# Kernel tuning notes

Hardware: AMD Instinct MI355X
Metric: run time of the kernel (lower is better)

## Reference

```python
import jax, jax.numpy as jnp
import numpy as np
import math

# Config constants (match init_kwargs)
E = 8          # n_experts
TOPK = 2       # attn_topk
DIM = 1024     # transformer_dim
B = 4          # batch_size
S = 1024       # max_seq_len
H = 1024       # num_heads * head_dim
SCALE = 1.0 / math.sqrt(DIM)  # original divides scores by sqrt(self.dim)


def setup_inputs() -> dict:
    key = jax.random.key(0)
    ks = jax.random.split(key, 8)
    w = 0.02  # weight init scale
    return {
        "X": jax.random.normal(ks[0], (B, S, DIM), jnp.float32),
        "mask": jnp.ones((B, S), jnp.float32),
        "switch_W": jax.random.normal(ks[1], (DIM * S, E), jnp.float32) * w,
        "switch_b": jnp.zeros((E,), jnp.float32),
        "Wq": jax.random.normal(ks[2], (E, DIM, H), jnp.float32) * w,
        "bq": jnp.zeros((E, H), jnp.float32),
        "Wk": jax.random.normal(ks[3], (E, DIM, H), jnp.float32) * w,
        "bk": jnp.zeros((E, H), jnp.float32),
        "Wv": jax.random.normal(ks[4], (E, DIM, H), jnp.float32) * w,
        "bv": jnp.zeros((E, H), jnp.float32),
        "Wff": jax.random.normal(ks[5], (E, H, DIM), jnp.float32) * w,
        "bff": jnp.zeros((E, DIM), jnp.float32),
    }


def _dispatch_mask(route_prob):
    # top-k expert routing per batch element -> hard {0,1} mask [B, E]
    _, idx = jax.lax.top_k(route_prob, TOPK)  # [B, TOPK]
    b = route_prob.shape[0]
    return jnp.zeros((b, E), route_prob.dtype).at[jnp.arange(b)[:, None], idx].set(1.0)


def reference(X, mask, switch_W, switch_b, Wq, bq, Wk, bk, Wv, bv, Wff, bff):
    b, s, d = X.shape
    # Router: Linear(dim*seq_len -> n_experts) + softmax; preprocess -> idx_list
    logits = X.reshape(b, -1) @ switch_W + switch_b          # [B, E]
    route_prob = jax.nn.softmax(logits, axis=-1)
    m = _dispatch_mask(route_prob)                            # [B, E] dispatch mask (idx_list)

    # Per-expert Q/K/V projections (ColumnParallelLinearWithMoE over routed batches)
    Q = jnp.einsum('bsd,edh->ebsh', X, Wq) + bq[:, None, None, :]  # [E,B,S,H]
    K = jnp.einsum('bsd,edh->ebsh', X, Wk) + bk[:, None, None, :]
    V = jnp.einsum('bsd,edh->ebsh', X, Wv) + bv[:, None, None, :]

    # RowParallelMatmulWithMoE: per-expert scores, softmax (dropout p=0)
    scores = jnp.einsum('ebsh,ebth->ebst', Q, K) * SCALE      # [E,B,S,S]
    P = jax.nn.softmax(scores, axis=-1)

    # index_add_ combine of per-expert attn maps (second preprocess reuses same routing)
    A = jnp.einsum('be,ebst->bst', m, P)                      # [B,S,S]

    # ColumnParallelMatmulWithMoE: attn @ V per expert
    ctx = jnp.einsum('bst,ebth->ebsh', A, V)                  # [E,B,S,H]

    # RowParallelLinearWithMoE output projection, then index_add_ combine
    out = jnp.einsum('ebsh,ehd->ebsd', ctx, Wff) + bff[:, None, None, :]
    y = jnp.einsum('be,ebsd->bsd', m, out)                    # [B,S,DIM]
    return y
```

## Files before the change

kernel.cpp:

```cpp
#include <hip/hip_runtime.h>
#include <math.h>

typedef unsigned short u16;
typedef __attribute__((ext_vector_type(8))) short bffrag;
typedef __attribute__((ext_vector_type(4))) float f32x4;
typedef __attribute__((ext_vector_type(4))) unsigned short us4;
typedef __attribute__((ext_vector_type(8))) unsigned short us8;

#define SCALE_QK (1.0f/32.0f)

__device__ __forceinline__ u16 f2bf(float f) {
    unsigned u = __builtin_bit_cast(unsigned, f);
    u += 0x7fffu + ((u >> 16) & 1u);
    return (u16)(u >> 16);
}

__device__ __forceinline__ void gld16(const u16* g, u16* l) {
    __builtin_amdgcn_global_load_lds(
        (const __attribute__((address_space(1))) void*)g,
        (__attribute__((address_space(3))) void*)l, 16, 0, 0);
}

__global__ __launch_bounds__(256) void router_partial(const float* __restrict__ X,
                                                      const float* __restrict__ sW,
                                                      float* __restrict__ part) {
    float acc[32];
    #pragma unroll
    for (int a = 0; a < 32; ++a) acc[a] = 0.f;
    int tid = blockIdx.x * 256 + threadIdx.x;
    #pragma unroll
    for (int q = 0; q < 4; ++q) {
        int i = tid + q * 262144;
        float4 w0 = *(const float4*)(sW + (size_t)i * 8);
        float4 w1 = *(const float4*)(sW + (size_t)i * 8 + 4);
        #pragma unroll
        for (int b = 0; b < 4; ++b) {
            float x = X[((size_t)b << 20) + i];
            acc[b*8+0] += x * w0.x; acc[b*8+1] += x * w0.y;
            acc[b*8+2] += x * w0.z; acc[b*8+3] += x * w0.w;
            acc[b*8+4] += x * w1.x; acc[b*8+5] += x * w1.y;
            acc[b*8+6] += x * w1.z; acc[b*8+7] += x * w1.w;
        }
    }
    __shared__ float wsum[4][32];
    int lane = threadIdx.x & 63, wv = threadIdx.x >> 6;
    #pragma unroll
    for (int a = 0; a < 32; ++a) {
        float v = acc[a];
        #pragma unroll
        for (int off = 32; off; off >>= 1) v += __shfl_down(v, off, 64);
        if (lane == 0) wsum[wv][a] = v;
    }
    __syncthreads();
    int t = threadIdx.x;
    if (t < 32)
        part[(size_t)t * 1024 + blockIdx.x] = wsum[0][t] + wsum[1][t] + wsum[2][t] + wsum[3][t];
}

__global__ __launch_bounds__(256) void router_final(const float* __restrict__ part,
                                                    const float* __restrict__ sb,
                                                    int* __restrict__ sel_need) {
    __shared__ float ps[32][8];
    __shared__ float lg[32];
    int t = threadIdx.x, a = t >> 3, c = t & 7;
    {
        float s = 0.f;
        const float* p = part + (size_t)a * 1024 + c * 128;
        for (int i = 0; i < 128; ++i) s += p[i];
        ps[a][c] = s;
    }
    __syncthreads();
    if (t < 32) {
        float v = 0.f;
        #pragma unroll
        for (int j = 0; j < 8; ++j) v += ps[t][j];
        lg[t] = v + sb[t & 7];
    }
    __syncthreads();
    if (t < 4) {
        int base = t * 8;
        int e1 = 0; float v1 = lg[base];
        for (int e = 1; e < 8; ++e) { if (lg[base + e] > v1) { v1 = lg[base + e]; e1 = e; } }
        int e2 = -1; float v2 = -INFINITY;
        for (int e = 0; e < 8; ++e) {
            if (e == e1) continue;
            if (lg[base + e] > v2) { v2 = lg[base + e]; e2 = e; }
        }
        sel_need[t * 2] = e1; sel_need[t * 2 + 1] = e2;
    }
    __syncthreads();
    if (t < 8) {
        int need = 0;
        for (int j = 0; j < 8; ++j) need |= (sel_need[j] == t);
        sel_need[8 + t] = need;
    }
}

__global__ __launch_bounds__(256) void c1_partial(const float* __restrict__ Wff,
        const float* __restrict__ bv, const int* __restrict__ sel_need,
        float* __restrict__ cpart) {
    int e = blockIdx.z;
    if (!sel_need[8 + e]) return;
    int d = blockIdx.x * 256 + threadIdx.x;
    int h0 = blockIdx.y * 128;
    const float* W = Wff + ((size_t)e << 20) + (size_t)h0 * 1024 + d;
    const float* bvp = bv + e * 1024 + h0;
    float s = 0.f;
    #pragma unroll 4
    for (int h = 0; h < 128; ++h) s += bvp[h] * W[(size_t)h * 1024];
    cpart[(e * 8 + blockIdx.y) * 1024 + d] = s;
}

__global__ __launch_bounds__(256) void ybias_kernel(const float* __restrict__ cpart,
        const float* __restrict__ bff, const int* __restrict__ sel,
        float* __restrict__ ybias) {
    int b = blockIdx.y;
    int d = blockIdx.x * 256 + threadIdx.x;
    int e0 = sel[b * 2], e1 = sel[b * 2 + 1];
    float c0 = 0.f, c1v = 0.f;
    #pragma unroll
    for (int hc = 0; hc < 8; ++hc) {
        c0  += cpart[(e0 * 8 + hc) * 1024 + d];
        c1v += cpart[(e1 * 8 + hc) * 1024 + d];
    }
    ybias[b * 1024 + d] = 2.f * (c0 + c1v) + bff[e0 * 1024 + d] + bff[e1 * 1024 + d];
}

__global__ __launch_bounds__(256) void cvt_misc(const float* __restrict__ X,
                                                const float* __restrict__ Wv,
                                                const int* __restrict__ sel_need,
                                                u16* __restrict__ Xb, u16* __restrict__ WvB) {
    int yz = blockIdx.y;
    const float* src; u16* dst;
    if (yz < 4) {
        src = X + ((size_t)yz << 20);  dst = Xb + ((size_t)yz << 20);
    } else {
        int e = yz - 4;
        if (!sel_need[8 + e]) return;
        src = Wv + ((size_t)e << 20);  dst = WvB + ((size_t)e << 20);
    }
    size_t i = (size_t)(blockIdx.x * 256 + threadIdx.x) * 8;
    float4 a = *(const float4*)(src + i);
    float4 b = *(const float4*)(src + i + 4);
    us8 o;
    o[0] = f2bf(a.x); o[1] = f2bf(a.y); o[2] = f2bf(a.z); o[3] = f2bf(a.w);
    o[4] = f2bf(b.x); o[5] = f2bf(b.y); o[6] = f2bf(b.z); o[7] = f2bf(b.w);
    *(us8*)(dst + i) = o;
}

__global__ __launch_bounds__(256) void cvt_wt(const float* __restrict__ Wq,
                                              const float* __restrict__ Wk,
                                              const float* __restrict__ Wff,
                                              const float* __restrict__ X,
                                              const int* __restrict__ sel_need,
                                              u16* __restrict__ WqT, u16* __restrict__ WkT,
                                              u16* __restrict__ WffT, u16* __restrict__ XbT) {
    int z = blockIdx.z;
    int type = z >> 3, e = z & 7;
    const float* src;
    u16* dst;
    if (type < 3) {
        if (!sel_need[8 + e]) return;
        src = (type == 0 ? Wq : type == 1 ? Wk : Wff) + ((size_t)e << 20);
        dst = (type == 0 ? WqT : type == 1 ? WkT : WffT) + ((size_t)e << 20);
    } else {
        int b = z & 3;
        src = X + ((size_t)b << 20);
        dst = XbT + ((size_t)b << 20);
    }
    __shared__ u16 lt[128 * 136];
    int R0 = blockIdx.y * 128, C0 = blockIdx.x * 128;
    int t = threadIdx.x;
    int c = t & 127;
    int rh = (t >> 7) * 4;
    #pragma unroll
    for (int it = 0; it < 16; ++it) {
        int r4 = it * 8 + rh;
        us4 o;
        #pragma unroll
        for (int j = 0; j < 4; ++j)
            o[j] = f2bf(src[(size_t)(R0 + r4 + j) * 1024 + C0 + c]);
        *(us4*)&lt[c * 136 + r4] = o;
    }
    __syncthreads();
    int dd = (t & 15) * 8;
    int hh = t >> 4;
    #pragma unroll
    for (int it = 0; it < 8; ++it) {
        int cr = it * 16 + hh;
        us8 o = *(const us8*)&lt[cr * 136 + dd];
        *(us8*)(dst + (size_t)(C0 + cr) * 1024 + R0 + dd) = o;
    }
}

__device__ __forceinline__ void stage_half8(const u16* g, int ld, u16* ldst, int tid) {
    int r = tid >> 3;
    int j = ((tid ^ r) & 7) * 8;
    gld16(g + (size_t)r * ld + j, ldst + tid * 8);
    gld16(g + (size_t)(r + 64) * ld + j, ldst + 4096 + tid * 8);
}

template<int Q, bool LASTVM>
__device__ __forceinline__ void phase8(const u16* Ac, const bffrag (&bfr)[4][2],
                                       f32x4 (&acc)[8][4], int rb, int l15, int x0,
                                       const u16* sg, int sld, u16* sdst, int tid) {
    bffrag af[2][2];
    #pragma unroll
    for (int mm = 0; mm < 2; ++mm) {
        int r = (rb + Q * 32 + mm * 16 + l15) * 64;
        af[mm][0] = *(const bffrag*)(Ac + r + x0);
        af[mm][1] = *(const bffrag*)(Ac + r + (x0 ^ 32));
    }
    __builtin_amdgcn_sched_barrier(0);
    stage_half8(sg, sld, sdst, tid);
    __builtin_amdgcn_sched_barrier(0);
    __builtin_amdgcn_s_barrier();
    asm volatile("s_waitcnt lgkmcnt(0)" ::: "memory");
    __builtin_amdgcn_sched_barrier(0);
    __builtin_amdgcn_s_setprio(1);
    #pragma unroll
    for (int ks = 0; ks < 2; ++ks)
        #pragma unroll
        for (int mm = 0; mm < 2; ++mm)
            #pragma unroll
            for (int nn = 0; nn < 4; ++nn)
                acc[Q*2+mm][nn] = __builtin_amdgcn_mfma_f32_16x16x32_bf16(
                    af[mm][ks], bfr[nn][ks], acc[Q*2+mm][nn], 0, 0, 0);
    __builtin_amdgcn_s_setprio(0);
    __builtin_amdgcn_sched_barrier(0);
    if (LASTVM) asm volatile("s_waitcnt vmcnt(4)" ::: "memory");
    __builtin_amdgcn_s_barrier();
}

__device__ __forceinline__ void gemm8(const u16* __restrict__ A, int lda,
                                      const u16* __restrict__ B, int ldb,
                                      int K, f32x4 (&acc)[8][4]) {
    __shared__ u16 lds[65536];
    const int tid = threadIdx.x, l = tid & 63, wid = tid >> 6;
    const int wr = wid >> 2, wc = wid & 3;
    const int l15 = l & 15;
    const int rb = wr * 128;
    const int cb = wc * 64;
    const int x0 = (((l >> 4) ^ (l & 7)) * 8);
    const int m0 = blockIdx.y * 256, n0 = blockIdx.x * 256;
    const int nt = K >> 6;

    const u16* Ag = A + (size_t)m0 * lda;
    const u16* Bg = B + (size_t)n0 * ldb;

    stage_half8(Ag,                          lda, lds,                 tid);
    stage_half8(Ag + (size_t)128 * lda,      lda, lds + 8192,          tid);
    stage_half8(Bg,                          ldb, lds + 16384,         tid);
    stage_half8(Bg + (size_t)128 * ldb,      ldb, lds + 16384 + 8192,  tid);
    stage_half8(Bg + 64,                     ldb, lds + 32768 + 16384, tid);
    stage_half8(Bg + 64 + (size_t)128 * ldb, ldb, lds + 32768 + 16384 + 8192, tid);
    asm volatile("s_waitcnt vmcnt(4)" ::: "memory");
    __builtin_amdgcn_s_barrier();

    for (int t7 = 0; t7 < nt; ++t7) {
        const int cur = t7 & 1;
        u16* Ac = lds + cur * 32768;
        u16* Bc = Ac + 16384;
        u16* An = lds + (cur ^ 1) * 32768;
        const int ka = (t7 + 1 < nt ? t7 + 1 : nt - 1) << 6;
        const int kb = (t7 + 2 < nt ? t7 + 2 : nt - 1) << 6;
        const u16* sA0 = Ag + ka;
        const u16* sA1 = Ag + (size_t)128 * lda + ka;
        const u16* sB0 = Bg + kb;
        const u16* sB1 = Bg + (size_t)128 * ldb + kb;

        bffrag bfr[4][2];
        #pragma unroll
        for (int nn = 0; nn < 4; ++nn) {
            int r = (cb + nn * 16 + l15) * 64;
            bfr[nn][0] = *(const bffrag*)(Bc + r + x0);
            bfr[nn][1] = *(const bffrag*)(Bc + r + (x0 ^ 32));
        }
        phase8<0, false>(Ac, bfr, acc, rb, l15, x0, sA0, lda, An, tid);
        phase8<1, false>(Ac, bfr, acc, rb, l15, x0, sA1, lda, An + 8192, tid);
        phase8<2, false>(Ac, bfr, acc, rb, l15, x0, sB0, ldb, Bc, tid);
        phase8<3, true >(Ac, bfr, acc, rb, l15, x0, sB1, ldb, Bc + 8192, tid);
    }
}

__device__ __forceinline__ void zero8(f32x4 (&acc)[8][4]) {
    #pragma unroll
    for (int m = 0; m < 8; ++m)
        #pragma unroll
        for (int n = 0; n < 4; ++n)
            #pragma unroll
            for (int i = 0; i < 4; ++i) acc[m][n][i] = 0.f;
}

__device__ __forceinline__ void epi8_bf16(u16* __restrict__ C, int ldc,
                                          const f32x4 (&acc)[8][4],
                                          const float* __restrict__ biasN) {
    const int tid = threadIdx.x, l = tid & 63, wid = tid >> 6;
    const int wr = wid >> 2, wc = wid & 3;
    const int m0 = blockIdx.y * 256 + wr * 128, n0 = blockIdx.x * 256 + wc * 64;
    const int l15 = l & 15, l4 = (l >> 4) * 4;
    #pragma unroll
    for (int mt = 0; mt < 8; ++mt)
        #pragma unroll
        for (int nn = 0; nn < 4; ++nn) {
            int col = n0 + nn * 16 + l15;
            float bn = biasN ? biasN[col] : 0.f;
            #pragma unroll
            for (int i = 0; i < 4; ++i) {
                int row = m0 + mt * 16 + l4 + i;
                C[(size_t)row * ldc + col] = f2bf(acc[mt][nn][i] + bn);
            }
        }
}

__device__ __forceinline__ void epi8_f32(float* __restrict__ C, int ldc, float scale,
                                         const f32x4 (&acc)[8][4]) {
    const int tid = threadIdx.x, l = tid & 63, wid = tid >> 6;
    const int wr = wid >> 2, wc = wid & 3;
    const int m0 = blockIdx.y * 256 + wr * 128, n0 = blockIdx.x * 256 + wc * 64;
    const int l15 = l & 15, l4 = (l >> 4) * 4;
    #pragma unroll
    for (int mt = 0; mt < 8; ++mt)
        #pragma unroll
        for (int nn = 0; nn < 4; ++nn) {
            int col = n0 + nn * 16 + l15;
            #pragma unroll
            for (int i = 0; i < 4; ++i) {
                int row = m0 + mt * 16 + l4 + i;
                C[(size_t)row * ldc + col] = acc[mt][nn][i] * scale;
            }
        }
}

__global__ __launch_bounds__(512) void mfma8_qk(const u16* __restrict__ Xb,
        const u16* __restrict__ WqT, const u16* __restrict__ WkT,
        const float* __restrict__ bq, const float* __restrict__ bk,
        const int* __restrict__ sel, u16* __restrict__ Qb, u16* __restrict__ Kb) {
    int z = blockIdx.z, w = z >> 3, bs = z & 7;
    int b = bs >> 1, e = sel[bs];
    f32x4 acc[8][4]; zero8(acc);
    gemm8(Xb + ((size_t)b << 20), 1024, (w ? WkT : WqT) + ((size_t)e << 20), 1024, 1024, acc);
    epi8_bf16((w ? Kb : Qb) + ((size_t)bs << 20), 1024, acc, (w ? bk : bq) + e * 1024);
}

__global__ __launch_bounds__(512) void mfma8_sw(const u16* __restrict__ Qb,
        const u16* __restrict__ Kb, const u16* __restrict__ WffT,
        const u16* __restrict__ WvB, const int* __restrict__ sel,
        float* __restrict__ S, float* __restrict__ P0, float* __restrict__ P1) {
    int z = blockIdx.z;
    f32x4 acc[8][4]; zero8(acc);
    if (z < 8) {
        gemm8(Qb + ((size_t)z << 20), 1024, Kb + ((size_t)z << 20), 1024, 1024, acc);
        epi8_f32(S + ((size_t)z << 20), 1024, SCALE_QK, acc);
    } else {
        int h = (z >= 12), b = z & 3, e = sel[b * 2 + h];
        gemm8(WffT + ((size_t)e << 20), 1024, WvB + ((size_t)e << 20), 1024, 1024, acc);
        epi8_f32((h ? P1 : P0) + ((size_t)b << 20), 1024, 1.0f, acc);
    }
}

__global__ __launch_bounds__(256) void wvfadd(const float* __restrict__ P0,
                                              const float* __restrict__ P1,
                                              u16* __restrict__ W) {
    size_t i = (size_t)(blockIdx.x * 256 + threadIdx.x) * 8;
    float4 a0 = *(const float4*)(P0 + i),     a1 = *(const float4*)(P0 + i + 4);
    float4 b0 = *(const float4*)(P1 + i),     b1 = *(const float4*)(P1 + i + 4);
    us8 o;
    o[0] = f2bf(a0.x + b0.x); o[1] = f2bf(a0.y + b0.y);
    o[2] = f2bf(a0.z + b0.z); o[3] = f2bf(a0.w + b0.w);
    o[4] = f2bf(a1.x + b1.x); o[5] = f2bf(a1.y + b1.y);
    o[6] = f2bf(a1.z + b1.z); o[7] = f2bf(a1.w + b1.w);
    *(us8*)(W + i) = o;
}

__device__ __forceinline__ void stage_tile(const u16* a0, const u16* a1,
                                           const u16* b0, const u16* b1,
                                           u16* sa, u16* sb, int tid) {
    gld16(a0, &sa[tid * 8]);
    gld16(a1, &sa[2048 + tid * 8]);
    gld16(b0, &sb[tid * 8]);
    gld16(b1, &sb[2048 + tid * 8]);
}

__device__ __forceinline__ void gemm_ds(const u16* __restrict__ A, int lda,
                                        const u16* __restrict__ B, int ldb,
                                        int K, f32x4 (&acc)[4][4]) {
    __shared__ u16 sA[2][4096];
    __shared__ u16 sB[2][4096];
    const int tid = threadIdx.x, lane = tid & 63, wv = tid >> 6;
    const int wr = (wv >> 1) * 64, wc = (wv & 1) * 64;
    const int l15 = lane & 15, lk = (lane >> 4) * 8;
    const int m0 = blockIdx.y * 128, n0 = blockIdx.x * 128;
    const int r0 = tid >> 2, k8 = (tid & 3) * 8;

    const u16* a0 = A + (size_t)(m0 + r0) * lda + k8;
    const u16* a1 = A + (size_t)(m0 + 64 + r0) * lda + k8;
    const u16* b0 = B + (size_t)(n0 + r0) * ldb + k8;
    const u16* b1 = B + (size_t)(n0 + 64 + r0) * ldb + k8;

    stage_tile(a0, a1, b0, b1, sA[0], sB[0], tid);
    __syncthreads();

    const int nt = K >> 5;
    for (int t = 0; t < nt; ++t) {
        const int cur = t & 1;
        if (t + 1 < nt) {
            int k0 = (t + 1) << 5;
            stage_tile(a0 + k0, a1 + k0, b0 + k0, b1 + k0, sA[cur ^ 1], sB[cur ^ 1], tid);
        }
        bffrag av[4], bf[4];
        #pragma unroll
        for (int m = 0; m < 4; ++m)
            av[m] = *reinterpret_cast<const bffrag*>(&sA[cur][(wr + m * 16 + l15) * 32 + lk]);
        #pragma unroll
        for (int n = 0; n < 4; ++n)
            bf[n] = *reinterpret_cast<const bffrag*>(&sB[cur][(wc + n * 16 + l15) * 32 + lk]);
        #pragma unroll
        for (int m = 0; m < 4; ++m)
            #pragma unroll
            for (int n = 0; n < 4; ++n)
                acc[m][n] = __builtin_amdgcn_mfma_f32_16x16x32_bf16(av[m], bf[n], acc[m][n], 0, 0, 0);
        __syncthreads();
    }
}

__device__ __forceinline__ void zero_acc(f32x4 (&acc)[4][4]) {
    #pragma unroll
    for (int m = 0; m < 4; ++m)
        #pragma unroll
        for (int n = 0; n < 4; ++n)
            #pragma unroll
            for (int i = 0; i < 4; ++i) acc[m][n][i] = 0.f;
}

__device__ __forceinline__ void epilogue_bf16(u16* __restrict__ C, int ldc,
                                              const f32x4 (&acc)[4][4]) {
    const int tid = threadIdx.x, lane = tid & 63, wv = tid >> 6;
    const int wr = (wv >> 1) * 64, wc = (wv & 1) * 64;
    const int m0 = blockIdx.y * 128, n0 = blockIdx.x * 128;
    const int l15 = lane & 15, l4 = (lane >> 4) * 4;
    #pragma unroll
    for (int m = 0; m < 4; ++m)
        #pragma unroll
        for (int n = 0; n < 4; ++n) {
            int col = n0 + wc + n * 16 + l15;
            #pragma unroll
            for (int i = 0; i < 4; ++i) {
                int row = m0 + wr + m * 16 + l4 + i;
                C[(size_t)row * ldc + col] = f2bf(acc[m][n][i]);
            }
        }
}

__device__ __forceinline__ void epilogue_f32(float* __restrict__ C, int ldc,
                                             const f32x4 (&acc)[4][4],
                                             const float* __restrict__ bias1) {
    const int tid = threadIdx.x, lane = tid & 63, wv = tid >> 6;
    const int wr = (wv >> 1) * 64, wc = (wv & 1) * 64;
    const int m0 = blockIdx.y * 128, n0 = blockIdx.x * 128;
    const int l15 = lane & 15, l4 = (lane >> 4) * 4;
    #pragma unroll
    for (int m = 0; m < 4; ++m)
        #pragma unroll
        for (int n = 0; n < 4; ++n) {
            int col = n0 + wc + n * 16 + l15;
            float bn = bias1 ? bias1[col] : 0.f;
            #pragma unroll
            for (int i = 0; i < 4; ++i) {
                int row = m0 + wr + m * 16 + l4 + i;
                C[(size_t)row * ldc + col] = acc[m][n][i] + bn;
            }
        }
}

__global__ __launch_bounds__(256) void sm_combine(const float* __restrict__ S, u16* __restrict__ Ab) {
    int bs = blockIdx.x, b = bs >> 10, s = bs & 1023;
    const float* S0 = S + ((size_t)(b * 2) << 20) + (size_t)s * 1024;
    const float* S1 = S0 + (1u << 20);
    int t = threadIdx.x, lane = t & 63, wv = t >> 6;
    float4 x0 = *(const float4*)(S0 + t * 4);
    float4 x1 = *(const float4*)(S1 + t * 4);
    float m0 = fmaxf(fmaxf(x0.x, x0.y), fmaxf(x0.z, x0.w));
    float m1 = fmaxf(fmaxf(x1.x, x1.y), fmaxf(x1.z, x1.w));
    #pragma unroll
    for (int off = 32; off; off >>= 1) {
        m0 = fmaxf(m0, __shfl_xor(m0, off, 64));
        m1 = fmaxf(m1, __shfl_xor(m1, off, 64));
    }
    __shared__ float wred[4][4];
    if (lane == 0) { wred[wv][0] = m0; wred[wv][1] = m1; }
    __syncthreads();
    m0 = fmaxf(fmaxf(wred[0][0], wred[1][0]), fmaxf(wred[2][0], wred[3][0]));
    m1 = fmaxf(fmaxf(wred[0][1], wred[1][1]), fmaxf(wred[2][1], wred[3][1]));
    float4 e0, e1;
    e0.x = __expf(x0.x - m0); e0.y = __expf(x0.y - m0); e0.z = __expf(x0.z - m0); e0.w = __expf(x0.w - m0);
    e1.x = __expf(x1.x - m1); e1.y = __expf(x1.y - m1); e1.z = __expf(x1.z - m1); e1.w = __expf(x1.w - m1);
    float s0 = e0.x + e0.y + e0.z + e0.w;
    float s1 = e1.x + e1.y + e1.z + e1.w;
    #pragma unroll
    for (int off = 32; off; off >>= 1) {
        s0 += __shfl_xor(s0, off, 64);
        s1 += __shfl_xor(s1, off, 64);
    }
    if (lane == 0) { wred[wv][2] = s0; wred[wv][3] = s1; }
    __syncthreads();
    s0 = wred[0][2] + wred[1][2] + wred[2][2] + wred[3][2];
    s1 = wred[0][3] + wred[1][3] + wred[2][3] + wred[3][3];
    float r0 = 1.f / s0, r1 = 1.f / s1;
    us4 o;
    o[0] = f2bf(e0.x * r0 + e1.x * r1); o[1] = f2bf(e0.y * r0 + e1.y * r1);
    o[2] = f2bf(e0.z * r0 + e1.z * r1); o[3] = f2bf(e0.w * r0 + e1.w * r1);
    *(us4*)(Ab + ((size_t)b << 20) + (size_t)s * 1024 + t * 4) = o;
}

__global__ __launch_bounds__(256) void mfma_ax(const u16* __restrict__ Abf,
        const u16* __restrict__ XbT, u16* __restrict__ AXbf) {
    int b = blockIdx.z;
    f32x4 acc[4][4]; zero_acc(acc);
    gemm_ds(Abf + ((size_t)b << 20), 1024, XbT + ((size_t)b << 20), 1024, 1024, acc);
    epilogue_bf16(AXbf + ((size_t)b << 20), 1024, acc);
}

__global__ __launch_bounds__(256) void mfma_y(const u16* __restrict__ AXbf,
        const u16* __restrict__ Wvfsum, const float* __restrict__ ybias,
        float* __restrict__ y) {
    int b = blockIdx.z;
    f32x4 acc[4][4]; zero_acc(acc);
    gemm_ds(AXbf + ((size_t)b << 20), 1024, Wvfsum + ((size_t)b << 20), 1024, 1024, acc);
    epilogue_f32(y + ((size_t)b << 20), 1024, acc, ybias + b * 1024);
}

extern "C" void kernel_launch(void* const* d_in, const int* in_sizes, int n_in,
                              void* d_out, int out_size, void* d_ws, size_t ws_size,
                              hipStream_t stream) {
    const float* X   = (const float*)d_in[0];
    const float* sW  = (const float*)d_in[2];
    const float* sb  = (const float*)d_in[3];
    const float* Wq  = (const float*)d_in[4];
    const float* bq  = (const float*)d_in[5];
    const float* Wk  = (const float*)d_in[6];
    const float* bk  = (const float*)d_in[7];
    const float* Wv  = (const float*)d_in[8];
    const float* bv  = (const float*)d_in[9];
    const float* Wff = (const float*)d_in[10];
    const float* bff = (const float*)d_in[11];
    float* y = (float*)d_out;

    char* w = (char*)d_ws;
    float* part  = (float*)w;
    float* cpart = (float*)w;
    int*   sel   = (int*)(w + (1u << 18));
    float* ybias = (float*)(w + (1u << 18) + 256);
    u16* base = (u16*)(w + (1u << 19));
    u16* Xb   = base;
    u16* XbT  = Xb   + (4u << 20);
    u16* WqT  = XbT  + (4u << 20);
    u16* WkT  = WqT  + (8u << 20);
    u16* WffT = WkT  + (8u << 20);
    u16* WvB  = WffT + (8u << 20);
    u16* Qb   = WvB  + (8u << 20);
    u16* Kb   = Qb   + (8u << 20);
    float* S  = (float*)(Kb + (8u << 20));
    float* P0 = S  + (8u << 20);
    float* P1 = P0 + (4u << 20);
    u16* Wvfsum = Xb;
    u16* Abf    = WqT;
    u16* AXbf   = WkT;

    router_partial<<<1024, 256, 0, stream>>>(X, sW, part);
    router_final<<<1, 256, 0, stream>>>(part, sb, sel);
    c1_partial<<<dim3(4, 8, 8), 256, 0, stream>>>(Wff, bv, sel, cpart);
    ybias_kernel<<<dim3(4, 4), 256, 0, stream>>>(cpart, bff, sel, ybias);
    cvt_misc<<<dim3(512, 12), 256, 0, stream>>>(X, Wv, sel, Xb, WvB);
    cvt_wt<<<dim3(8, 8, 28), 256, 0, stream>>>(Wq, Wk, Wff, X, sel, WqT, WkT, WffT, XbT);

    mfma8_qk<<<dim3(4, 4, 16), 512, 0, stream>>>(Xb, WqT, WkT, bq, bk, sel, Qb, Kb);
    mfma8_sw<<<dim3(4, 4, 16), 512, 0, stream>>>(Qb, Kb, WffT, WvB, sel, S, P0, P1);
    wvfadd<<<2048, 256, 0, stream>>>(P0, P1, Wvfsum);
    sm_combine<<<4096, 256, 0, stream>>>(S, Abf);
    mfma_ax<<<dim3(8, 8, 4), 256, 0, stream>>>(Abf, XbT, AXbf);
    mfma_y<<<dim3(8, 8, 4), 256, 0, stream>>>(AXbf, Wvfsum, ybias, y);
}
```

Baseline: 239.1 us.

## Reassociate A·X·Wvf product, store scores/partials in bf16, drop X transpose

Reorders the final product from (A·X)·Wvfsum to A·(X·Wvfsum)^T-style by computing a per-batch Mt = Wvfsum·X first. That removes the need for a transposed bf16 copy of X, so the cvt_wt grid shrinks. Score matrices and the Wff·Wv partial products are now written as bf16 instead of fp32, halving their store and reload traffic in softmax and wvfadd. In exchange the scores are rounded to bf16 before softmax, which costs accuracy.

Result: faster. 221.8 us (-7.2%).

```diff
diff --git a/kernel.cpp b/kernel.cpp
--- a/kernel.cpp
+++ b/kernel.cpp
@@ -13,6 +13,10 @@
     unsigned u = __builtin_bit_cast(unsigned, f);
     u += 0x7fffu + ((u >> 16) & 1u);
     return (u16)(u >> 16);
+}
+__device__ __forceinline__ float bf2f(u16 v) {
+    unsigned u = ((unsigned)v) << 16;
+    return __builtin_bit_cast(float, u);
 }
 
 __device__ __forceinline__ void gld16(const u16* g, u16* l) {
@@ -151,23 +155,14 @@
 __global__ __launch_bounds__(256) void cvt_wt(const float* __restrict__ Wq,
                                               const float* __restrict__ Wk,
                                               const float* __restrict__ Wff,
-                                              const float* __restrict__ X,
                                               const int* __restrict__ sel_need,
                                               u16* __restrict__ WqT, u16* __restrict__ WkT,
-                                              u16* __restrict__ WffT, u16* __restrict__ XbT) {
+                                              u16* __restrict__ WffT) {
     int z = blockIdx.z;
     int type = z >> 3, e = z & 7;
-    const float* src;
-    u16* dst;
-    if (type < 3) {
-        if (!sel_need[8 + e]) return;
-        src = (type == 0 ? Wq : type == 1 ? Wk : Wff) + ((size_t)e << 20);
-        dst = (type == 0 ? WqT : type == 1 ? WkT : WffT) + ((size_t)e << 20);
-    } else {
-        int b = z & 3;
-        src = X + ((size_t)b << 20);
-        dst = XbT + ((size_t)b << 20);
-    }
+    if (!sel_need[8 + e]) return;
+    const float* src = (type == 0 ? Wq : type == 1 ? Wk : Wff) + ((size_t)e << 20);
+    u16* dst = (type == 0 ? WqT : type == 1 ? WkT : WffT) + ((size_t)e << 20);
     __shared__ u16 lt[128 * 136];
     int R0 = blockIdx.y * 128, C0 = blockIdx.x * 128;
     int t = threadIdx.x;
@@ -292,7 +287,7 @@
             for (int i = 0; i < 4; ++i) acc[m][n][i] = 0.f;
 }
 
-__device__ __forceinline__ void epi8_bf16(u16* __restrict__ C, int ldc,
+__device__ __forceinline__ void epi8_bf16(u16* __restrict__ C, int ldc, float scale,
                                           const f32x4 (&acc)[8][4],
                                           const float* __restrict__ biasN) {
     const int tid = threadIdx.x, l = tid & 63, wid = tid >> 6;
@@ -308,26 +303,7 @@
             #pragma unroll
             for (int i = 0; i < 4; ++i) {
                 int row = m0 + mt * 16 + l4 + i;
-                C[(size_t)row * ldc + col] = f2bf(acc[mt][nn][i] + bn);
-            }
-        }
-}
-
-__device__ __forceinline__ void epi8_f32(float* __restrict__ C, int ldc, float scale,
-                                         const f32x4 (&acc)[8][4]) {
-    const int tid = threadIdx.x, l = tid & 63, wid = tid >> 6;
-    const int wr = wid >> 2, wc = wid & 3;
-    const int m0 = blockIdx.y * 256 + wr * 128, n0 = blockIdx.x * 256 + wc * 64;
-    const int l15 = l & 15, l4 = (l >> 4) * 4;
-    #pragma unroll
-    for (int mt = 0; mt < 8; ++mt)
-        #pragma unroll
-        for (int nn = 0; nn < 4; ++nn) {
-            int col = n0 + nn * 16 + l15;
-            #pragma unroll
-            for (int i = 0; i < 4; ++i) {
-                int row = m0 + mt * 16 + l4 + i;
-                C[(size_t)row * ldc + col] = acc[mt][nn][i] * scale;
+                C[(size_t)row * ldc + col] = f2bf(acc[mt][nn][i] * scale + bn);
             }
         }
 }
@@ -340,36 +316,34 @@
     int b = bs >> 1, e = sel[bs];
     f32x4 acc[8][4]; zero8(acc);
     gemm8(Xb + ((size_t)b << 20), 1024, (w ? WkT : WqT) + ((size_t)e << 20), 1024, 1024, acc);
-    epi8_bf16((w ? Kb : Qb) + ((size_t)bs << 20), 1024, acc, (w ? bk : bq) + e * 1024);
+    epi8_bf16((w ? Kb : Qb) + ((size_t)bs << 20), 1024, 1.0f, acc, (w ? bk : bq) + e * 1024);
 }
 
 __global__ __launch_bounds__(512) void mfma8_sw(const u16* __restrict__ Qb,
         const u16* __restrict__ Kb, const u16* __restrict__ WffT,
         const u16* __restrict__ WvB, const int* __restrict__ sel,
-        float* __restrict__ S, float* __restrict__ P0, float* __restrict__ P1) {
+        u16* __restrict__ Sb, u16* __restrict__ P0b, u16* __restrict__ P1b) {
     int z = blockIdx.z;
     f32x4 acc[8][4]; zero8(acc);
     if (z < 8) {
         gemm8(Qb + ((size_t)z << 20), 1024, Kb + ((size_t)z << 20), 1024, 1024, acc);
-        epi8_f32(S + ((size_t)z << 20), 1024, SCALE_QK, acc);
+        epi8_bf16(Sb + ((size_t)z << 20), 1024, SCALE_QK, acc, nullptr);
     } else {
         int h = (z >= 12), b = z & 3, e = sel[b * 2 + h];
         gemm8(WffT + ((size_t)e << 20), 1024, WvB + ((size_t)e << 20), 1024, 1024, acc);
-        epi8_f32((h ? P1 : P0) + ((size_t)b << 20), 1024, 1.0f, acc);
-    }
-}
-
-__global__ __launch_bounds__(256) void wvfadd(const float* __restrict__ P0,
-                                              const float* __restrict__ P1,
+        epi8_bf16((h ? P1b : P0b) + ((size_t)b << 20), 1024, 1.0f, acc, nullptr);
+    }
+}
+
+__global__ __launch_bounds__(256) void wvfadd(const u16* __restrict__ P0b,
+                                              const u16* __restrict__ P1b,
                                               u16* __restrict__ W) {
     size_t i = (size_t)(blockIdx.x * 256 + threadIdx.x) * 8;
-    float4 a0 = *(const float4*)(P0 + i),     a1 = *(const float4*)(P0 + i + 4);
-    float4 b0 = *(const float4*)(P1 + i),     b1 = *(const float4*)(P1 + i + 4);
+    us8 a = *(const us8*)(P0b + i);
+    us8 b = *(const us8*)(P1b + i);
     us8 o;
-    o[0] = f2bf(a0.x + b0.x); o[1] = f2bf(a0.y + b0.y);
-    o[2] = f2bf(a0.z + b0.z); o[3] = f2bf(a0.w + b0.w);
-    o[4] = f2bf(a1.x + b1.x); o[5] = f2bf(a1.y + b1.y);
-    o[6] = f2bf(a1.z + b1.z); o[7] = f2bf(a1.w + b1.w);
+    #pragma unroll
+    for (int j = 0; j < 8; ++j) o[j] = f2bf(bf2f(a[j]) + bf2f(b[j]));
     *(us8*)(W + i) = o;
 }
 
@@ -473,15 +447,18 @@
         }
 }
 
-__global__ __launch_bounds__(256) void sm_combine(const float* __restrict__ S, u16* __restrict__ Ab) {
+__global__ __launch_bounds__(256) void sm_combine(const u16* __restrict__ Sb, u16* __restrict__ Ab) {
     int bs = blockIdx.x, b = bs >> 10, s = bs & 1023;
-    const float* S0 = S + ((size_t)(b * 2) << 20) + (size_t)s * 1024;
-    const float* S1 = S0 + (1u << 20);
+    const u16* S0 = Sb + ((size_t)(b * 2) << 20) + (size_t)s * 1024;
+    const u16* S1 = S0 + (1u << 20);
     int t = threadIdx.x, lane = t & 63, wv = t >> 6;
-    float4 x0 = *(const float4*)(S0 + t * 4);
-    float4 x1 = *(const float4*)(S1 + t * 4);
-    float m0 = fmaxf(fmaxf(x0.x, x0.y), fmaxf(x0.z, x0.w));
-    float m1 = fmaxf(fmaxf(x1.x, x1.y), fmaxf(x1.z, x1.w));
+    us4 xv0 = *(const us4*)(S0 + t * 4);
+    us4 xv1 = *(const us4*)(S1 + t * 4);
+    float x0[4], x1[4];
+    #pragma unroll
+    for (int j = 0; j < 4; ++j) { x0[j] = bf2f(xv0[j]); x1[j] = bf2f(xv1[j]); }
+    float m0 = fmaxf(fmaxf(x0[0], x0[1]), fmaxf(x0[2], x0[3]));
+    float m1 = fmaxf(fmaxf(x1[0], x1[1]), fmaxf(x1[2], x1[3]));
     #pragma unroll
     for (int off = 32; off; off >>= 1) {
         m0 = fmaxf(m0, __shfl_xor(m0, off, 64));
@@ -492,11 +469,11 @@
     __syncthreads();
     m0 = fmaxf(fmaxf(wred[0][0], wred[1][0]), fmaxf(wred[2][0], wred[3][0]));
     m1 = fmaxf(fmaxf(wred[0][1], wred[1][1]), fmaxf(wred[2][1], wred[3][1]));
-    float4 e0, e1;
-    e0.x = __expf(x0.x - m0); e0.y = __expf(x0.y - m0); e0.z = __expf(x0.z - m0); e0.w = __expf(x0.w - m0);
-    e1.x = __expf(x1.x - m1); e1.y = __expf(x1.y - m1); e1.z = __expf(x1.z - m1); e1.w = __expf(x1.w - m1);
-    float s0 = e0.x + e0.y + e0.z + e0.w;
-    float s1 = e1.x + e1.y + e1.z + e1.w;
+    float e0[4], e1[4];
+    #pragma unroll
+    for (int j = 0; j < 4; ++j) { e0[j] = __expf(x0[j] - m0); e1[j] = __expf(x1[j] - m1); }
+    float s0 = e0[0] + e0[1] + e0[2] + e0[3];
+    float s1 = e1[0] + e1[1] + e1[2] + e1[3];
     #pragma unroll
     for (int off = 32; off; off >>= 1) {
         s0 += __shfl_xor(s0, off, 64);
@@ -508,25 +485,25 @@
     s1 = wred[0][3] + wred[1][3] + wred[2][3] + wred[3][3];
     float r0 = 1.f / s0, r1 = 1.f / s1;
     us4 o;
-    o[0] = f2bf(e0.x * r0 + e1.x * r1); o[1] = f2bf(e0.y * r0 + e1.y * r1);
-    o[2] = f2bf(e0.z * r0 + e1.z * r1); o[3] = f2bf(e0.w * r0 + e1.w * r1);
+    #pragma unroll
+    for (int j = 0; j < 4; ++j) o[j] = f2bf(e0[j] * r0 + e1[j] * r1);
     *(us4*)(Ab + ((size_t)b << 20) + (size_t)s * 1024 + t * 4) = o;
 }
 
-__global__ __launch_bounds__(256) void mfma_ax(const u16* __restrict__ Abf,
-        const u16* __restrict__ XbT, u16* __restrict__ AXbf) {
+__global__ __launch_bounds__(256) void mfma_mt(const u16* __restrict__ Wvfsum,
+        const u16* __restrict__ Xb, u16* __restrict__ Mtb) {
     int b = blockIdx.z;
     f32x4 acc[4][4]; zero_acc(acc);
-    gemm_ds(Abf + ((size_t)b << 20), 1024, XbT + ((size_t)b << 20), 1024, 1024, acc);
-    epilogue_bf16(AXbf + ((size_t)b << 20), 1024, acc);
-}
-
-__global__ __launch_bounds__(256) void mfma_y(const u16* __restrict__ AXbf,
-        const u16* __restrict__ Wvfsum, const float* __restrict__ ybias,
+    gemm_ds(Wvfsum + ((size_t)b << 20), 1024, Xb + ((size_t)b << 20), 1024, 1024, acc);
+    epilogue_bf16(Mtb + ((size_t)b << 20), 1024, acc);
+}
+
+__global__ __launch_bounds__(256) void mfma_y(const u16* __restrict__ Abf,
+        const u16* __restrict__ Mtb, const float* __restrict__ ybias,
         float* __restrict__ y) {
     int b = blockIdx.z;
     f32x4 acc[4][4]; zero_acc(acc);
-    gemm_ds(AXbf + ((size_t)b << 20), 1024, Wvfsum + ((size_t)b << 20), 1024, 1024, acc);
+    gemm_ds(Abf + ((size_t)b << 20), 1024, Mtb + ((size_t)b << 20), 1024, 1024, acc);
     epilogue_f32(y + ((size_t)b << 20), 1024, acc, ybias + b * 1024);
 }
 
@@ -553,31 +530,30 @@
     float* ybias = (float*)(w + (1u << 18) + 256);
     u16* base = (u16*)(w + (1u << 19));
     u16* Xb   = base;
-    u16* XbT  = Xb   + (4u << 20);
-    u16* WqT  = XbT  + (4u << 20);
+    u16* WqT  = Xb   + (4u << 20);
     u16* WkT  = WqT  + (8u << 20);
     u16* WffT = WkT  + (8u << 20);
     u16* WvB  = WffT + (8u << 20);
     u16* Qb   = WvB  + (8u << 20);
     u16* Kb   = Qb   + (8u << 20);
-    float* S  = (float*)(Kb + (8u << 20));
-    float* P0 = S  + (8u << 20);
-    float* P1 = P0 + (4u << 20);
-    u16* Wvfsum = Xb;
+    u16* Sb   = Kb   + (8u << 20);
+    u16* P0b  = Sb   + (8u << 20);
+    u16* P1b  = P0b  + (4u << 20);
     u16* Abf    = WqT;
-    u16* AXbf   = WkT;
+    u16* Mtb    = WkT;
+    u16* Wvfsum = Qb;
 
     router_partial<<<1024, 256, 0, stream>>>(X, sW, part);
     router_final<<<1, 256, 0, stream>>>(part, sb, sel);
     c1_partial<<<dim3(4, 8, 8), 256, 0, stream>>>(Wff, bv, sel, cpart);
     ybias_kernel<<<dim3(4, 4), 256, 0, stream>>>(cpart, bff, sel, ybias);
     cvt_misc<<<dim3(512, 12), 256, 0, stream>>>(X, Wv, sel, Xb, WvB);
-    cvt_wt<<<dim3(8, 8, 28), 256, 0, stream>>>(Wq, Wk, Wff, X, sel, WqT, WkT, WffT, XbT);
+    cvt_wt<<<dim3(8, 8, 24), 256, 0, stream>>>(Wq, Wk, Wff, sel, WqT, WkT, WffT);
 
     mfma8_qk<<<dim3(4, 4, 16), 512, 0, stream>>>(Xb, WqT, WkT, bq, bk, sel, Qb, Kb);
-    mfma8_sw<<<dim3(4, 4, 16), 512, 0, stream>>>(Qb, Kb, WffT, WvB, sel, S, P0, P1);
-    wvfadd<<<2048, 256, 0, stream>>>(P0, P1, Wvfsum);
-    sm_combine<<<4096, 256, 0, stream>>>(S, Abf);
-    mfma_ax<<<dim3(8, 8, 4), 256, 0, stream>>>(Abf, XbT, AXbf);
-    mfma_y<<<dim3(8, 8, 4), 256, 0, stream>>>(AXbf, Wvfsum, ybias, y);
-}
+    mfma8_sw<<<dim3(4, 4, 16), 512, 0, stream>>>(Qb, Kb, WffT, WvB, sel, Sb, P0b, P1b);
+    wvfadd<<<2048, 256, 0, stream>>>(P0b, P1b, Wvfsum);
+    mfma_mt<<<dim3(8, 8, 4), 256, 0, stream>>>(Wvfsum, Xb, Mtb);
+    sm_combine<<<4096, 256, 0, stream>>>(Sb, Abf);
+    mfma_y<<<dim3(8, 8, 4), 256, 0, stream>>>(Abf, Mtb, ybias, y);
+}
```
